# Performance work log

Measured on AMD Instinct MI355X. Metric: run time of the kernel, lower is better.

Reference implementation:

```python
import jax, jax.numpy as jnp
import numpy as np

B, S, D, H = 2, 2048, 1024, 16
DK = D // H  # 64


def setup_inputs() -> dict:
    key = jax.random.key(0)
    ks = jax.random.split(key, 8)
    q = jax.random.normal(ks[0], (B, S, D), dtype=jnp.float32)
    k = jax.random.normal(ks[1], (B, S, D), dtype=jnp.float32)
    v = jax.random.normal(ks[2], (B, S, D), dtype=jnp.float32)
    mask = jax.random.randint(ks[3], (B, 1, S, S), 0, 2, dtype=jnp.int32)
    scale = 1.0 / np.sqrt(D)
    Wq = jax.random.normal(ks[4], (D, D), dtype=jnp.float32) * scale
    Wk = jax.random.normal(ks[5], (D, D), dtype=jnp.float32) * scale
    Wv = jax.random.normal(ks[6], (D, D), dtype=jnp.float32) * scale
    Wo = jax.random.normal(ks[7], (D, D), dtype=jnp.float32) * scale
    return {"q": q, "k": k, "v": v, "mask": mask,
            "Wq": Wq, "Wk": Wk, "Wv": Wv, "Wo": Wo}


def reference(q, k, v, mask, Wq, Wk, Wv, Wo):
    # Linear projections (torch nn.Linear: x @ W.T, no bias)
    qh = (q @ Wq.T).reshape(B, S, H, DK).transpose(0, 2, 1, 3)  # [B,H,S,DK]
    kh = (k @ Wk.T).reshape(B, S, H, DK).transpose(0, 2, 1, 3)
    vh = (v @ Wv.T).reshape(B, S, H, DK).transpose(0, 2, 1, 3)
    # Scaled dot-product attention with mask fill of -1e9 where mask == 0
    scores = jnp.einsum('bhqd,bhkd->bhqk', qh, kh) / jnp.sqrt(jnp.float32(DK))
    scores = jnp.where(mask == 0, jnp.float32(-1e9), scores)
    attn = jax.nn.softmax(scores, axis=-1)
    ctx = jnp.einsum('bhqk,bhkd->bhqd', attn, vh)  # [B,H,S,DK]
    ctx = ctx.transpose(0, 2, 1, 3).reshape(B, S, D)
    return ctx @ Wo.T
```

## Files before the change

### kernel.cpp

```cpp
#include <hip/hip_runtime.h>

using u16    = unsigned short;
using u32    = unsigned int;
using f32x4  = __attribute__((ext_vector_type(4))) float;
using f32x16 = __attribute__((ext_vector_type(16))) float;
using bf16x8 = __attribute__((ext_vector_type(8))) __bf16;
using u16x4  = __attribute__((ext_vector_type(4))) u16;
using u16x8  = __attribute__((ext_vector_type(8))) u16;
using u32x2  = __attribute__((ext_vector_type(2))) u32;
using u32x4  = __attribute__((ext_vector_type(4))) u32;
using i32x4  = __attribute__((ext_vector_type(4))) int;


__device__ __forceinline__ u16 f2bf(float f) {
  union { __bf16 b; u16 u; } c; c.b = (__bf16)f; return c.u;
}

typedef __attribute__((address_space(1))) const void GVoid;
typedef __attribute__((address_space(3))) void LVoid;

__device__ __forceinline__ void gload_lds16(const void* g, void* l) {
  __builtin_amdgcn_global_load_lds((GVoid*)g, (LVoid*)l, 16, 0, 0);
}

__global__ void cvt_w(const float* __restrict__ a, const float* __restrict__ b,
                      const float* __restrict__ c, const float* __restrict__ dd,
                      u16* __restrict__ oa, u16* __restrict__ ob,
                      u16* __restrict__ oc, u16* __restrict__ od) {
  int y = blockIdx.y;
  const float* s = (y == 0) ? a : (y == 1) ? b : (y == 2) ? c : dd;
  u16* d = (y == 0) ? oa : (y == 1) ? ob : (y == 2) ? oc : od;
  int i = blockIdx.x * 256 + threadIdx.x;
  f32x4 v = ((const f32x4*)s)[i];
  u16x4 r;
#pragma unroll
  for (int j = 0; j < 4; ++j) r[j] = f2bf(v[j]);
  ((u16x4*)d)[i] = r;
}

__global__ void pack_mask(const int* __restrict__ m, u32* __restrict__ mp) {
  int tid = blockIdx.x * 256 + threadIdx.x;
  int q = tid & 2047, kt = (tid >> 11) & 31, b = tid >> 16;
  const i32x4* src = (const i32x4*)(m + ((size_t)(b * 2048 + q)) * 2048 + kt * 64);
  u32 w0 = 0, w1 = 0;
#pragma unroll
  for (int j = 0; j < 8; ++j) {
    i32x4 a = src[j], c = src[j + 8];
#pragma unroll
    for (int e = 0; e < 4; ++e) {
      w0 |= (a[e] != 0 ? 1u : 0u) << (j * 4 + e);
      w1 |= (c[e] != 0 ? 1u : 0u) << (j * 4 + e);
    }
  }
  ((u32x2*)mp)[((size_t)(b * 32 + kt)) * 2048 + q] = u32x2{w0, w1};
}

__global__ __launch_bounds__(256, 2) void gemm_qkv(const float* __restrict__ Aq,
                                                   const float* __restrict__ Ak,
                                                   const float* __restrict__ Av,
                                                   const u16* __restrict__ Wb,
                                                   u16* __restrict__ out) {
  __shared__ alignas(16) char lds[49152];
  const int t = threadIdx.x;
  const int lane = t & 63, wid = t >> 6;
  const int g = lane >> 4, r16 = lane & 15;
  const int wm = wid >> 1, wn = wid & 1;
  const int m0 = blockIdx.x * 128, n0 = blockIdx.y * 128;
  const int z = blockIdx.z;

  const float* Axf = (z == 0) ? Aq : (z == 1) ? Ak : Av;
  const char* Ab = (const char*)Axf;
  const char* Bb = (const char*)(Wb + (size_t)z * 1048576);
  u16* op = out + (size_t)z * 4194304;
  const float qsc = (z == 0) ? 0.18033688011f : 1.0f;

  f32x4 acc[4][4] = {};

  for (int kk = 0; kk < 1024; kk += 64) {
#pragma unroll
    for (int i = 0; i < 8; ++i) {
      int ci = i * 256 + t;
      int row = ci >> 4;
      int pc = ci & 15;
      int lc = pc ^ (row & 15);
      gload_lds16(Ab + (size_t)(m0 + row) * 4096 + kk * 4 + lc * 16, lds + ci * 16);
    }
#pragma unroll
    for (int i = 0; i < 4; ++i) {
      int ci = i * 256 + t;
      int row = ci >> 3;
      int cbs = ((ci & 7) << 4) ^ ((row & 7) << 4);
      gload_lds16(Bb + (size_t)(n0 + row) * 2048 + kk * 2 + cbs, lds + 32768 + ci * 16);
    }
    __syncthreads();
#pragma unroll
    for (int kc = 0; kc < 2; ++kc) {
      bf16x8 af[4], bfr[4];
#pragma unroll
      for (int mf = 0; mf < 4; ++mf) {
        int row = wm * 64 + mf * 16 + r16;
        const char* arow = lds + row * 256;
        int x = row & 15;
        int lc0 = 8 * kc + 2 * g;
        f32x4 alo = *(const f32x4*)(arow + ((lc0 ^ x) * 16));
        f32x4 ahi = *(const f32x4*)(arow + (((lc0 + 1) ^ x) * 16));
        u16x8 pk;
#pragma unroll
        for (int j = 0; j < 4; ++j) { pk[j] = f2bf(alo[j]); pk[4 + j] = f2bf(ahi[j]); }
        af[mf] = __builtin_bit_cast(bf16x8, pk);
      }
#pragma unroll
      for (int nf = 0; nf < 4; ++nf) {
        int row = wn * 64 + nf * 16 + r16;
        bfr[nf] = *(const bf16x8*)(lds + 32768 + row * 128 +
                                   ((64 * kc + 16 * g) ^ ((row & 7) << 4)));
      }
#pragma unroll
      for (int mf = 0; mf < 4; ++mf)
#pragma unroll
        for (int nf = 0; nf < 4; ++nf)
          acc[mf][nf] = __builtin_amdgcn_mfma_f32_16x16x32_bf16(af[mf], bfr[nf], acc[mf][nf], 0, 0, 0);
    }
    __syncthreads();
  }

#pragma unroll
  for (int mf = 0; mf < 4; ++mf) {
#pragma unroll
    for (int nf = 0; nf < 4; ++nf) {
      int mb = m0 + wm * 64 + mf * 16 + 4 * g;
      int n = n0 + wn * 64 + nf * 16 + r16;
      if (z == 0) {
        int bb = mb >> 11, h = n >> 6, dk = n & 63;
#pragma unroll
        for (int r = 0; r < 4; ++r) {
          int s2 = (mb + r) & 2047;
          op[((size_t)(bb * 16 + h) * 2048 + s2) * 64 + dk] = f2bf(acc[mf][nf][r] * qsc);
        }
      } else if (z == 1) {
        int h = n >> 6, dk = n & 63;
#pragma unroll
        for (int r = 0; r < 4; ++r) {
          int m = mb + r;
          int bb = m >> 11, s2 = m & 2047;
          size_t off16 = ((((size_t)(bb * 16 + h) * 32 + (s2 >> 6)) * 2 + ((s2 >> 5) & 1)) * 8 +
                          (dk >> 3)) * 32 + (s2 & 31);
          op[off16 * 8 + (dk & 7)] = f2bf(acc[mf][nf][r]);
        }
      } else {
        int bb = mb >> 11, s2 = mb & 2047, h = n >> 6, d = n & 63;
        size_t off16 = ((((size_t)(bb * 16 + h) * 32 + (s2 >> 6)) * 8 + ((s2 & 63) >> 3)) * 2 +
                        (d >> 5)) * 32 + (d & 31);
        u16x4 pv;
#pragma unroll
        for (int r = 0; r < 4; ++r) pv[r] = f2bf(acc[mf][nf][r]);
        *(u16x4*)(op + off16 * 8 + (s2 & 7)) = pv;
      }
    }
  }
}

__global__ __launch_bounds__(256, 2) void gemm_out(const u16* __restrict__ X,
                                                   const u16* __restrict__ W,
                                                   float* __restrict__ out) {
  __shared__ alignas(16) char lds[32768];
  const int t = threadIdx.x;
  const int lane = t & 63, wid = t >> 6;
  const int g = lane >> 4, r16 = lane & 15;
  const int wm = wid >> 1, wn = wid & 1;
  const int m0 = blockIdx.x * 128, n0 = blockIdx.y * 128;
  const char* Ab = (const char*)X;
  const char* Bb = (const char*)W;

  f32x4 acc[4][4] = {};

  for (int kk = 0; kk < 1024; kk += 64) {
#pragma unroll
    for (int i = 0; i < 4; ++i) {
      int ci = i * 256 + t;
      int row = ci >> 3;
      int cbs = ((ci & 7) << 4) ^ ((row & 7) << 4);
      gload_lds16(Ab + (size_t)(m0 + row) * 2048 + kk * 2 + cbs, lds + ci * 16);
      gload_lds16(Bb + (size_t)(n0 + row) * 2048 + kk * 2 + cbs, lds + 16384 + ci * 16);
    }
    __syncthreads();
#pragma unroll
    for (int kc = 0; kc < 2; ++kc) {
      bf16x8 af[4], bfr[4];
#pragma unroll
      for (int mf = 0; mf < 4; ++mf) {
        int row = wm * 64 + mf * 16 + r16;
        af[mf] = *(const bf16x8*)(lds + row * 128 + ((64 * kc + 16 * g) ^ ((row & 7) << 4)));
      }
#pragma unroll
      for (int nf = 0; nf < 4; ++nf) {
        int row = wn * 64 + nf * 16 + r16;
        bfr[nf] = *(const bf16x8*)(lds + 16384 + row * 128 + ((64 * kc + 16 * g) ^ ((row & 7) << 4)));
      }
#pragma unroll
      for (int mf = 0; mf < 4; ++mf)
#pragma unroll
        for (int nf = 0; nf < 4; ++nf)
          acc[mf][nf] = __builtin_amdgcn_mfma_f32_16x16x32_bf16(af[mf], bfr[nf], acc[mf][nf], 0, 0, 0);
    }
    __syncthreads();
  }

#pragma unroll
  for (int mf = 0; mf < 4; ++mf)
#pragma unroll
    for (int nf = 0; nf < 4; ++nf) {
      int mb = m0 + wm * 64 + mf * 16 + 4 * g;
      int n = n0 + wn * 64 + nf * 16 + r16;
#pragma unroll
      for (int r = 0; r < 4; ++r) out[(size_t)(mb + r) * 1024 + n] = acc[mf][nf][r];
    }
}

struct KF { bf16x8 k0[4], k1[4]; };

__device__ __forceinline__ void loadK(KF& f, const char* p) {
#pragma unroll
  for (int c = 0; c < 4; ++c) {
    f.k0[c] = *(const bf16x8*)(p + c * 1024);
    f.k1[c] = *(const bf16x8*)(p + 4096 + c * 1024);
  }
}

__device__ __forceinline__ void attn_body(const bf16x8 (&qf)[4], KF& cur, KF& nxt,
                                          const char*& kp, const char*& vp0,
                                          const char*& vp1, const u32x2*& mptr,
                                          u32x2& mcur, int hi,
                                          f32x16& o0, f32x16& o1, float& l_run) {
  bf16x8 v0[4], v1[4];
#pragma unroll
  for (int ks = 0; ks < 4; ++ks) {
    v0[ks] = *(const bf16x8*)(vp0 + ks * 2048);
    v1[ks] = *(const bf16x8*)(vp1 + ks * 2048);
  }
  loadK(nxt, kp);
  u32x2 mnext = *mptr;
  kp += 8192; vp0 += 8192; vp1 += 8192; mptr += 2048;
  __builtin_amdgcn_sched_barrier(0);

  f32x16 s0 = {}, s1 = {};
#pragma unroll
  for (int c = 0; c < 4; ++c) {
    s0 = __builtin_amdgcn_mfma_f32_32x32x16_bf16(cur.k0[c], qf[c], s0, 0, 0, 0);
    s1 = __builtin_amdgcn_mfma_f32_32x32x16_bf16(cur.k1[c], qf[c], s1, 0, 0, 0);
  }

  u32 wa = mcur.x >> (4 * hi), wb = mcur.y >> (4 * hi);
  float ps = 0.f;
#pragma unroll
  for (int r = 0; r < 16; ++r) {
    const int bit = (r & 3) + 8 * (r >> 2);
    float p0 = __builtin_amdgcn_exp2f(s0[r]);
    float p1 = __builtin_amdgcn_exp2f(s1[r]);
    int sm0 = ((int)(wa << (31 - bit))) >> 31;
    int sm1 = ((int)(wb << (31 - bit))) >> 31;
    p0 = __uint_as_float(__float_as_uint(p0) & (u32)sm0);
    p1 = __uint_as_float(__float_as_uint(p1) & (u32)sm1);
    s0[r] = p0; s1[r] = p1;
    ps += p0 + p1;
  }
  l_run += ps;

  u32 w[16];
#pragma unroll
  for (int kb = 0; kb < 2; ++kb) {
#pragma unroll
    for (int ss = 0; ss < 2; ++ss) {
      const f32x16& sp = kb ? s1 : s0;
      u32 A0, B0, A1, B1;
      asm("v_cvt_pk_bf16_f32 %0, %1, %2" : "=v"(A0) : "v"(sp[8*ss+0]), "v"(sp[8*ss+1]));
      asm("v_cvt_pk_bf16_f32 %0, %1, %2" : "=v"(B0) : "v"(sp[8*ss+2]), "v"(sp[8*ss+3]));
      asm("v_cvt_pk_bf16_f32 %0, %1, %2" : "=v"(A1) : "v"(sp[8*ss+4]), "v"(sp[8*ss+5]));
      asm("v_cvt_pk_bf16_f32 %0, %1, %2" : "=v"(B1) : "v"(sp[8*ss+6]), "v"(sp[8*ss+7]));
      asm("v_permlane32_swap_b32 %0, %1" : "+v"(A0), "+v"(A1));
      asm("v_permlane32_swap_b32 %0, %1" : "+v"(B0), "+v"(B1));
      int f = 2 * kb + ss;
      w[4*f+0] = A0; w[4*f+1] = B0; w[4*f+2] = A1; w[4*f+3] = B1;
    }
  }

#pragma unroll
  for (int ks = 0; ks < 4; ++ks) {
    bf16x8 pa = __builtin_bit_cast(bf16x8, u32x4{w[4*ks], w[4*ks+1], w[4*ks+2], w[4*ks+3]});
    o0 = __builtin_amdgcn_mfma_f32_32x32x16_bf16(pa, v0[ks], o0, 0, 0, 0);
    o1 = __builtin_amdgcn_mfma_f32_32x32x16_bf16(pa, v1[ks], o1, 0, 0, 0);
  }
  mcur = mnext;
}

__global__ __launch_bounds__(256, 2) void attn_kern(const u16* __restrict__ Qh,
                                                    const u16* __restrict__ Kh,
                                                    const u16* __restrict__ Vt,
                                                    const u32* __restrict__ mp,
                                                    u16* __restrict__ ctx) {
  __shared__ float cmb[2][32][64];
  __shared__ float cmbl[2][64];
  const int t = threadIdx.x;
  const int wid = t >> 6, lane = t & 63;
  const int qw = wid & 1, kh = wid >> 1;
  const int hi = lane >> 5, l31 = lane & 31;

  const int wg = (blockIdx.x & 7) * 128 + (blockIdx.x >> 3);
  const int qt = wg & 31, bh = wg >> 5;
  const int b = bh >> 4, h = bh & 15;

  const char* qbytes = (const char*)Qh;
  const int qbase = qt * 64 + qw * 32;
  const int qg = qbase + l31;

  bf16x8 qf[4];
#pragma unroll
  for (int c = 0; c < 4; ++c)
    qf[c] = *(const bf16x8*)(qbytes + ((size_t)bh * 2048 + qg) * 128 + 32 * c + 16 * hi);

  const char* kp  = (const char*)Kh + (size_t)bh * 262144 + (size_t)kh * 131072 + hi * 512 + l31 * 16;
  const char* vp0 = (const char*)Vt + (size_t)bh * 262144 + (size_t)kh * 131072 + hi * 1024 + l31 * 16;
  const char* vp1 = vp0 + 512;
  const u32x2* mptr = (const u32x2*)mp + (size_t)b * 65536 + (size_t)kh * 32768 + qg;

  f32x16 o0 = {}, o1 = {};
  float l_run = 0.f;

  KF A, B2;
  loadK(A, kp);
  kp += 8192;
  u32x2 mcur = *mptr;
  mptr += 2048;

#pragma unroll 1
  for (int it = 0; it < 8; ++it) {
    attn_body(qf, A, B2, kp, vp0, vp1, mptr, mcur, hi, o0, o1, l_run);
    attn_body(qf, B2, A, kp, vp0, vp1, mptr, mcur, hi, o0, o1, l_run);
  }

  l_run += __shfl_xor(l_run, 32, 64);

  if (kh) {
#pragma unroll
    for (int r = 0; r < 16; ++r) {
      cmb[qw][r][lane]      = o0[r];
      cmb[qw][16 + r][lane] = o1[r];
    }
    cmbl[qw][lane] = l_run;
  }
  __syncthreads();
  if (!kh) {
#pragma unroll
    for (int r = 0; r < 16; ++r) {
      o0[r] += cmb[qw][r][lane];
      o1[r] += cmb[qw][16 + r][lane];
    }
    l_run += cmbl[qw][lane];

    float rl = 1.f / l_run;
#pragma unroll
    for (int r = 0; r < 16; ++r) {
      float rv = __shfl(rl, (r & 3) + 8 * (r >> 2) + 4 * hi, 64);
      int q = qbase + (r & 3) + 8 * (r >> 2) + 4 * hi;
      size_t rowp = ((size_t)b * 2048 + q) * 1024 + h * 64 + l31;
      ctx[rowp]      = f2bf(o0[r] * rv);
      ctx[rowp + 32] = f2bf(o1[r] * rv);
    }
  }
}

extern "C" void kernel_launch(void* const* d_in, const int* in_sizes, int n_in,
                              void* d_out, int out_size, void* d_ws, size_t ws_size,
                              hipStream_t stream) {
  const float* q  = (const float*)d_in[0];
  const float* k  = (const float*)d_in[1];
  const float* v  = (const float*)d_in[2];
  const int* mask = (const int*)d_in[3];
  const float* Wq = (const float*)d_in[4];
  const float* Wk = (const float*)d_in[5];
  const float* Wv = (const float*)d_in[6];
  const float* Wo = (const float*)d_in[7];

  u16* ws = (u16*)d_ws;
  const size_t NX = (size_t)4096 * 1024;
  const size_t NW = (size_t)1024 * 1024;
  u16* Wqb = ws + 3 * NX;
  u16* Qh  = Wqb + 4 * NW;
  u16* ctx = Qh + 3 * NX;
  u32* mpk = (u32*)ws;

  cvt_w<<<dim3(1024, 4), 256, 0, stream>>>(Wq, Wk, Wv, Wo,
                                           Wqb, Wqb + NW, Wqb + 2 * NW, Wqb + 3 * NW);
  pack_mask<<<dim3(512), 256, 0, stream>>>(mask, mpk);
  gemm_qkv<<<dim3(32, 8, 3), 256, 0, stream>>>(q, k, v, Wqb, Qh);
  attn_kern<<<dim3(1024), 256, 0, stream>>>(Qh, Qh + NX, Qh + 2 * NX, mpk, ctx);
  gemm_out<<<dim3(32, 8), 256, 0, stream>>>(ctx, Wqb + 3 * NW, (float*)d_out);
}
```

Before: 125.9 us.

## Double-buffer QKV projection LDS tiles with prefetch of next K-slice

Result: no change. 128.1 us (+1.7%).

```diff
diff --git a/kernel.cpp b/kernel.cpp
--- a/kernel.cpp
+++ b/kernel.cpp
@@ -76,53 +76,68 @@
 
   f32x4 acc[4][4] = {};
 
-  for (int kk = 0; kk < 1024; kk += 64) {
-#pragma unroll
-    for (int i = 0; i < 8; ++i) {
-      int ci = i * 256 + t;
-      int row = ci >> 4;
-      int pc = ci & 15;
-      int lc = pc ^ (row & 15);
-      gload_lds16(Ab + (size_t)(m0 + row) * 4096 + kk * 4 + lc * 16, lds + ci * 16);
-    }
-#pragma unroll
-    for (int i = 0; i < 4; ++i) {
-      int ci = i * 256 + t;
-      int row = ci >> 3;
-      int cbs = ((ci & 7) << 4) ^ ((row & 7) << 4);
-      gload_lds16(Bb + (size_t)(n0 + row) * 2048 + kk * 2 + cbs, lds + 32768 + ci * 16);
-    }
-    __syncthreads();
-#pragma unroll
-    for (int kc = 0; kc < 2; ++kc) {
-      bf16x8 af[4], bfr[4];
-#pragma unroll
-      for (int mf = 0; mf < 4; ++mf) {
-        int row = wm * 64 + mf * 16 + r16;
-        const char* arow = lds + row * 256;
-        int x = row & 15;
-        int lc0 = 8 * kc + 2 * g;
-        f32x4 alo = *(const f32x4*)(arow + ((lc0 ^ x) * 16));
-        f32x4 ahi = *(const f32x4*)(arow + (((lc0 + 1) ^ x) * 16));
-        u16x8 pk;
-#pragma unroll
-        for (int j = 0; j < 4; ++j) { pk[j] = f2bf(alo[j]); pk[4 + j] = f2bf(ahi[j]); }
-        af[mf] = __builtin_bit_cast(bf16x8, pk);
-      }
-#pragma unroll
-      for (int nf = 0; nf < 4; ++nf) {
-        int row = wn * 64 + nf * 16 + r16;
-        bfr[nf] = *(const bf16x8*)(lds + 32768 + row * 128 +
-                                   ((64 * kc + 16 * g) ^ ((row & 7) << 4)));
-      }
-#pragma unroll
-      for (int mf = 0; mf < 4; ++mf)
-#pragma unroll
-        for (int nf = 0; nf < 4; ++nf)
-          acc[mf][nf] = __builtin_amdgcn_mfma_f32_16x16x32_bf16(af[mf], bfr[nf], acc[mf][nf], 0, 0, 0);
-    }
-    __syncthreads();
-  }
+#define STAGEG(BUF, KK)                                                         \
+  {                                                                             \
+    char* base = lds + (BUF) * 24576;                                           \
+    _Pragma("unroll") for (int i = 0; i < 4; ++i) {          \
+      int ci = i * 256 + t;                                                     \
+      int row = ci >> 3;                                                        \
+      int lc = (ci & 7) ^ (row & 7);                                            \
+      gload_lds16(Ab + (size_t)(m0 + row) * 4096 + (KK) * 4 + lc * 16,          \
+                  base + ci * 16);                                              \
+    }                                                                           \
+    _Pragma("unroll") for (int i = 0; i < 2; ++i) {           \
+      int ci = i * 256 + t;                                                     \
+      int row = ci >> 2;                                                        \
+      int lc = (ci & 3) ^ ((row >> 1) & 3);                                     \
+      gload_lds16(Bb + (size_t)(n0 + row) * 2048 + (KK) * 2 + lc * 16,          \
+                  base + 16384 + ci * 16);                                      \
+    }                                                                           \
+  }
+
+  STAGEG(0, 0);
+
+#pragma unroll 1
+  for (int kt = 0; kt < 32; ++kt) {
+    const char* cb = lds + (kt & 1) * 24576;
+    if (kt < 31) {
+      STAGEG((kt + 1) & 1, (kt + 1) * 32);
+      asm volatile("s_waitcnt vmcnt(6)" ::: "memory");
+    } else {
+      asm volatile("s_waitcnt vmcnt(0)" ::: "memory");
+    }
+    __builtin_amdgcn_s_barrier();
+    asm volatile("" ::: "memory");
+
+    bf16x8 af[4], bfr[4];
+#pragma unroll
+    for (int mf = 0; mf < 4; ++mf) {
+      int row = wm * 64 + mf * 16 + r16;
+      const char* arow = cb + row * 128;
+      int x = row & 7;
+      f32x4 alo = *(const f32x4*)(arow + (((2 * g) ^ x) * 16));
+      f32x4 ahi = *(const f32x4*)(arow + (((2 * g + 1) ^ x) * 16));
+      u16x8 pk;
+#pragma unroll
+      for (int j = 0; j < 4; ++j) { pk[j] = f2bf(alo[j]); pk[4 + j] = f2bf(ahi[j]); }
+      af[mf] = __builtin_bit_cast(bf16x8, pk);
+    }
+#pragma unroll
+    for (int nf = 0; nf < 4; ++nf) {
+      int row = wn * 64 + nf * 16 + r16;
+      bfr[nf] = *(const bf16x8*)(cb + 16384 + row * 64 + ((g ^ ((row >> 1) & 3)) * 16));
+    }
+#pragma unroll
+    for (int mf = 0; mf < 4; ++mf)
+#pragma unroll
+      for (int nf = 0; nf < 4; ++nf)
+        acc[mf][nf] = __builtin_amdgcn_mfma_f32_16x16x32_bf16(af[mf], bfr[nf], acc[mf][nf], 0, 0, 0);
+
+    asm volatile("" ::: "memory");
+    __builtin_amdgcn_s_barrier();
+    asm volatile("" ::: "memory");
+  }
+#undef STAGEG
 
 #pragma unroll
   for (int mf = 0; mf < 4; ++mf) {
```

## Split attention tile into two half passes to cut registers and raise occupancy

Applied to the files above, without the earlier changes.

After: 143.8 us. +14.2%, slower.

```diff
diff --git a/kernel.cpp b/kernel.cpp
--- a/kernel.cpp
+++ b/kernel.cpp
@@ -227,73 +227,72 @@
   }
 }
 
+__device__ __forceinline__ void half_pass(const bf16x8 (&qf)[4], const bf16x8 (&kh)[4],
+                                          const char* vp0, const char* vp1, int ksbase,
+                                          u32 wmask, float (&psx)[4],
+                                          f32x16& o0, f32x16& o1) {
+  bf16x8 va0 = *(const bf16x8*)(vp0 + (ksbase + 0) * 2048);
+  bf16x8 va1 = *(const bf16x8*)(vp0 + (ksbase + 1) * 2048);
+  bf16x8 vb0 = *(const bf16x8*)(vp1 + (ksbase + 0) * 2048);
+  bf16x8 vb1 = *(const bf16x8*)(vp1 + (ksbase + 1) * 2048);
+
+  f32x16 s = {};
+#pragma unroll
+  for (int c = 0; c < 4; ++c)
+    s = __builtin_amdgcn_mfma_f32_32x32x16_bf16(kh[c], qf[c], s, 0, 0, 0);
+
+#pragma unroll
+  for (int r = 0; r < 16; ++r) {
+    const int bit = (r & 3) + 8 * (r >> 2);
+    float p = __builtin_amdgcn_exp2f(s[r]);
+    int sm;
+    asm("v_bfe_i32 %0, %1, %2, 1" : "=v"(sm) : "v"(wmask), "i"(bit));
+    p = __uint_as_float(__float_as_uint(p) & (u32)sm);
+    s[r] = p;
+    psx[r & 3] += p;
+  }
+
+  u32 w[8];
+#pragma unroll
+  for (int ss = 0; ss < 2; ++ss) {
+    u32 A0, B0, A1, B1;
+    asm("v_cvt_pk_bf16_f32 %0, %1, %2" : "=v"(A0) : "v"(s[8*ss+0]), "v"(s[8*ss+1]));
+    asm("v_cvt_pk_bf16_f32 %0, %1, %2" : "=v"(B0) : "v"(s[8*ss+2]), "v"(s[8*ss+3]));
+    asm("v_cvt_pk_bf16_f32 %0, %1, %2" : "=v"(A1) : "v"(s[8*ss+4]), "v"(s[8*ss+5]));
+    asm("v_cvt_pk_bf16_f32 %0, %1, %2" : "=v"(B1) : "v"(s[8*ss+6]), "v"(s[8*ss+7]));
+    asm("v_permlane32_swap_b32 %0, %1" : "+v"(A0), "+v"(A1));
+    asm("v_permlane32_swap_b32 %0, %1" : "+v"(B0), "+v"(B1));
+    w[4*ss+0] = A0; w[4*ss+1] = B0; w[4*ss+2] = A1; w[4*ss+3] = B1;
+  }
+
+  bf16x8 pa0 = __builtin_bit_cast(bf16x8, u32x4{w[0], w[1], w[2], w[3]});
+  bf16x8 pa1 = __builtin_bit_cast(bf16x8, u32x4{w[4], w[5], w[6], w[7]});
+  o0 = __builtin_amdgcn_mfma_f32_32x32x16_bf16(pa0, va0, o0, 0, 0, 0);
+  o1 = __builtin_amdgcn_mfma_f32_32x32x16_bf16(pa0, vb0, o1, 0, 0, 0);
+  o0 = __builtin_amdgcn_mfma_f32_32x32x16_bf16(pa1, va1, o0, 0, 0, 0);
+  o1 = __builtin_amdgcn_mfma_f32_32x32x16_bf16(pa1, vb1, o1, 0, 0, 0);
+}
+
 __device__ __forceinline__ void attn_body(const bf16x8 (&qf)[4], KF& cur, KF& nxt,
                                           const char*& kp, const char*& vp0,
                                           const char*& vp1, const u32x2*& mptr,
                                           u32x2& mcur, int hi,
                                           f32x16& o0, f32x16& o1, float& l_run) {
-  bf16x8 v0[4], v1[4];
-#pragma unroll
-  for (int ks = 0; ks < 4; ++ks) {
-    v0[ks] = *(const bf16x8*)(vp0 + ks * 2048);
-    v1[ks] = *(const bf16x8*)(vp1 + ks * 2048);
-  }
   loadK(nxt, kp);
   u32x2 mnext = *mptr;
-  kp += 8192; vp0 += 8192; vp1 += 8192; mptr += 2048;
+  kp += 8192; mptr += 2048;
   __builtin_amdgcn_sched_barrier(0);
 
-  f32x16 s0 = {}, s1 = {};
-#pragma unroll
-  for (int c = 0; c < 4; ++c) {
-    s0 = __builtin_amdgcn_mfma_f32_32x32x16_bf16(cur.k0[c], qf[c], s0, 0, 0, 0);
-    s1 = __builtin_amdgcn_mfma_f32_32x32x16_bf16(cur.k1[c], qf[c], s1, 0, 0, 0);
-  }
-
-  u32 wa = mcur.x >> (4 * hi), wb = mcur.y >> (4 * hi);
-  float ps = 0.f;
-#pragma unroll
-  for (int r = 0; r < 16; ++r) {
-    const int bit = (r & 3) + 8 * (r >> 2);
-    float p0 = __builtin_amdgcn_exp2f(s0[r]);
-    float p1 = __builtin_amdgcn_exp2f(s1[r]);
-    int sm0 = ((int)(wa << (31 - bit))) >> 31;
-    int sm1 = ((int)(wb << (31 - bit))) >> 31;
-    p0 = __uint_as_float(__float_as_uint(p0) & (u32)sm0);
-    p1 = __uint_as_float(__float_as_uint(p1) & (u32)sm1);
-    s0[r] = p0; s1[r] = p1;
-    ps += p0 + p1;
-  }
-  l_run += ps;
-
-  u32 w[16];
-#pragma unroll
-  for (int kb = 0; kb < 2; ++kb) {
-#pragma unroll
-    for (int ss = 0; ss < 2; ++ss) {
-      const f32x16& sp = kb ? s1 : s0;
-      u32 A0, B0, A1, B1;
-      asm("v_cvt_pk_bf16_f32 %0, %1, %2" : "=v"(A0) : "v"(sp[8*ss+0]), "v"(sp[8*ss+1]));
-      asm("v_cvt_pk_bf16_f32 %0, %1, %2" : "=v"(B0) : "v"(sp[8*ss+2]), "v"(sp[8*ss+3]));
-      asm("v_cvt_pk_bf16_f32 %0, %1, %2" : "=v"(A1) : "v"(sp[8*ss+4]), "v"(sp[8*ss+5]));
-      asm("v_cvt_pk_bf16_f32 %0, %1, %2" : "=v"(B1) : "v"(sp[8*ss+6]), "v"(sp[8*ss+7]));
-      asm("v_permlane32_swap_b32 %0, %1" : "+v"(A0), "+v"(A1));
-      asm("v_permlane32_swap_b32 %0, %1" : "+v"(B0), "+v"(B1));
-      int f = 2 * kb + ss;
-      w[4*f+0] = A0; w[4*f+1] = B0; w[4*f+2] = A1; w[4*f+3] = B1;
-    }
-  }
-
-#pragma unroll
-  for (int ks = 0; ks < 4; ++ks) {
-    bf16x8 pa = __builtin_bit_cast(bf16x8, u32x4{w[4*ks], w[4*ks+1], w[4*ks+2], w[4*ks+3]});
-    o0 = __builtin_amdgcn_mfma_f32_32x32x16_bf16(pa, v0[ks], o0, 0, 0, 0);
-    o1 = __builtin_amdgcn_mfma_f32_32x32x16_bf16(pa, v1[ks], o1, 0, 0, 0);
-  }
+  float psx[4] = {0.f, 0.f, 0.f, 0.f};
+  half_pass(qf, cur.k0, vp0, vp1, 0, mcur.x >> (4 * hi), psx, o0, o1);
+  half_pass(qf, cur.k1, vp0, vp1, 2, mcur.y >> (4 * hi), psx, o0, o1);
+  l_run += (psx[0] + psx[1]) + (psx[2] + psx[3]);
+
+  vp0 += 8192; vp1 += 8192;
   mcur = mnext;
 }
 
-__global__ __launch_bounds__(256, 2) void attn_kern(const u16* __restrict__ Qh,
+__global__ __launch_bounds__(256, 3) void attn_kern(const u16* __restrict__ Qh,
                                                     const u16* __restrict__ Kh,
                                                     const u16* __restrict__ Vt,
                                                     const u32* __restrict__ mp,
```
